# Kernel tuning notes

Hardware: AMD Instinct MI355X
Metric: run time of the kernel (lower is better)

Reference implementation:

```python
import jax, jax.numpy as jnp
import numpy as np

NUM_ITERS = 5
TEMP = 0.1


def setup_inputs() -> dict:
    key = jax.random.key(0)
    k1, k2 = jax.random.split(key)
    pred_masks = jax.random.uniform(k1, (1, 100, 512, 512), dtype=jnp.float32)
    gt_masks = jax.random.uniform(k2, (50, 512, 512), dtype=jnp.float32)
    return {"pred_masks": pred_masks, "gt_masks": gt_masks}


def reference(pred_masks, gt_masks):
    # pred_masks: [B=1, K, H, W]; gt_masks: [N, H, W]
    gt = gt_masks[None]  # [1, N, H, W]
    # cost[b,k,n] = 1 - <pred_k, gt_n> over HW
    cost = 1.0 - jnp.einsum('bkhw,bnhw->bkn', pred_masks, gt)
    log_alpha = -cost / TEMP  # [1, K, N]
    for _ in range(NUM_ITERS):
        log_alpha = log_alpha - jax.nn.logsumexp(log_alpha, axis=2, keepdims=True)
        log_alpha = log_alpha - jax.nn.logsumexp(log_alpha, axis=1, keepdims=True)
    return jnp.exp(log_alpha)
```

## Files before the change

kernel.cpp:

```cpp
#include <hip/hip_runtime.h>
#include <math.h>

#define HW    262144
#define MROWS 100
#define NCOLS 50
#define OUTSZ (MROWS * NCOLS)

typedef __attribute__((ext_vector_type(8))) short bf16x8;
typedef __attribute__((ext_vector_type(4))) float f32x4;

__device__ __forceinline__ unsigned short f32_bf16(float x) {
  unsigned int u = __float_as_uint(x);
  u += 0x7FFFu + ((u >> 16) & 1u);
  return (unsigned short)(u >> 16);
}
__device__ __forceinline__ float bf16_f32(unsigned short h) {
  return __uint_as_float(((unsigned int)h) << 16);
}
__device__ __forceinline__ void split_frag(const float4& v0, const float4& v1,
                                           bf16x8& hi, bf16x8& lo) {
  float xs[8] = {v0.x, v0.y, v0.z, v0.w, v1.x, v1.y, v1.z, v1.w};
#pragma unroll
  for (int j = 0; j < 8; ++j) {
    unsigned short h = f32_bf16(xs[j]);
    hi[j] = (short)h;
    lo[j] = (short)f32_bf16(xs[j] - bf16_f32(h));
  }
}

#define ABYTES   14336
#define BUFBYTES 24576
#define SLOT_ITERS 6

typedef __attribute__((address_space(1))) const unsigned int GU32;
typedef __attribute__((address_space(3))) unsigned int LU32;

__global__ __launch_bounds__(256, 3) void dm_phase1(
    const float* __restrict__ pred, const float* __restrict__ gt,
    float* __restrict__ partial, int chunk) {
  __shared__ unsigned char smem[2 * BUFBYTES];

  const int b    = blockIdx.x;
  const int tid  = threadIdx.x;
  const int lane = tid & 63;
  const int wid  = tid >> 6;
  const int wi = wid >> 1, wj = wid & 1;
  const int g = lane >> 4, r = lane & 15;

  const int kbase = b * chunk;
  const int nst   = chunk >> 5;

  const float* srcb[SLOT_ITERS];
#pragma unroll
  for (int it = 0; it < SLOT_ITERS; ++it) {
    int s = it * 256 + tid;
    if (s < 896) {
      int row = s >> 3, t = s & 7;
      int rr = row < MROWS ? row : MROWS - 1;
      srcb[it] = pred + (size_t)rr * HW + ((t ^ (row & 7)) << 2);
    } else if (s < 1408) {
      int s2 = s - 896;
      int row = s2 >> 3, t = s2 & 7;
      int rr = row < NCOLS ? row : NCOLS - 1;
      srcb[it] = gt + (size_t)rr * HW + ((t ^ (row & 7)) << 2);
    } else {
      srcb[it] = pred + ((s - 1408) << 2);
    }
  }

  auto STAGE = [&](int q, int k0f) {
    unsigned char* bufb = smem + q * BUFBYTES;
#pragma unroll
    for (int it = 0; it < SLOT_ITERS; ++it) {
      const float* src = srcb[it] + k0f;
      unsigned char* dst = bufb + (it * 256 + wid * 64) * 16;
      __builtin_amdgcn_global_load_lds((GU32*)src, (LU32*)dst, 16, 0, 0);
    }
  };

  f32x4 acc[4][2] = {};

  auto COMPUTE = [&](int q) {
    const unsigned char* bufb = smem + q * BUFBYTES;
    bf16x8 bh[2], bl[2];
#pragma unroll
    for (int nf = 0; nf < 2; ++nf) {
      int R = wj * 32 + nf * 16 + r;
      const unsigned char* rowb = bufb + ABYTES + R * 128;
      float4 v0 = *(const float4*)(rowb + (((2 * g    ) ^ (r & 7)) << 4));
      float4 v1 = *(const float4*)(rowb + (((2 * g + 1) ^ (r & 7)) << 4));
      split_frag(v0, v1, bh[nf], bl[nf]);
    }
#pragma unroll
    for (int mf = 0; mf < 4; ++mf) {
      if (wi == 0 || mf < 3) {
        int R = wi * 64 + mf * 16 + r;
        const unsigned char* rowb = bufb + R * 128;
        float4 v0 = *(const float4*)(rowb + (((2 * g    ) ^ (r & 7)) << 4));
        float4 v1 = *(const float4*)(rowb + (((2 * g + 1) ^ (r & 7)) << 4));
        bf16x8 ah, al;
        split_frag(v0, v1, ah, al);
#pragma unroll
        for (int nf = 0; nf < 2; ++nf) {
          acc[mf][nf] = __builtin_amdgcn_mfma_f32_16x16x32_bf16(ah, bh[nf], acc[mf][nf], 0, 0, 0);
          acc[mf][nf] = __builtin_amdgcn_mfma_f32_16x16x32_bf16(al, bh[nf], acc[mf][nf], 0, 0, 0);
          acc[mf][nf] = __builtin_amdgcn_mfma_f32_16x16x32_bf16(ah, bl[nf], acc[mf][nf], 0, 0, 0);
          acc[mf][nf] = __builtin_amdgcn_mfma_f32_16x16x32_bf16(al, bl[nf], acc[mf][nf], 0, 0, 0);
        }
      }
    }
  };

  STAGE(0, kbase);
  for (int s = 0; s < nst; ++s) {
    asm volatile("s_barrier" ::: "memory");
    if (s + 1 < nst) {
      STAGE((s + 1) & 1, kbase + (s + 1) * 32);
      asm volatile("s_waitcnt vmcnt(6)" ::: "memory");
    } else {
      asm volatile("s_waitcnt vmcnt(0)" ::: "memory");
    }
    asm volatile("s_barrier" ::: "memory");
    COMPUTE(s & 1);
  }

#pragma unroll
  for (int mf = 0; mf < 4; ++mf) {
#pragma unroll
    for (int nf = 0; nf < 2; ++nf) {
#pragma unroll
      for (int qq = 0; qq < 4; ++qq) {
        int row = wi * 64 + mf * 16 + g * 4 + qq;
        int col = wj * 32 + nf * 16 + r;
        if (row < MROWS && col < NCOLS)
          partial[(size_t)b * OUTSZ + row * NCOLS + col] = acc[mf][nf][qq];
      }
    }
  }
}

__global__ void dm_reduce(const float* __restrict__ partial,
                          double* __restrict__ la0, int nblk) {
  const int tid = threadIdx.x, wid = tid >> 6, lane = tid & 63;
  const int pbase = blockIdx.x * 16 + wid * 4;
  if (pbase >= OUTSZ) return;
  double d0 = 0, d1 = 0, d2 = 0, d3 = 0;
  for (int b = lane; b < nblk; b += 64) {
    float4 v = *(const float4*)(partial + (size_t)b * OUTSZ + pbase);
    d0 += (double)v.x; d1 += (double)v.y; d2 += (double)v.z; d3 += (double)v.w;
  }
#pragma unroll
  for (int off = 32; off; off >>= 1) {
    d0 += __shfl_xor(d0, off);
    d1 += __shfl_xor(d1, off);
    d2 += __shfl_xor(d2, off);
    d3 += __shfl_xor(d3, off);
  }
  if (lane == 0) {
    la0[pbase + 0] = (d0 - 1.0) * 10.0;
    la0[pbase + 1] = (d1 - 1.0) * 10.0;
    la0[pbase + 2] = (d2 - 1.0) * 10.0;
    la0[pbase + 3] = (d3 - 1.0) * 10.0;
  }
}

__global__ __launch_bounds__(256) void dm_sinkhorn(const double* __restrict__ la_in,
                                                   float* __restrict__ out) {
  __shared__ double la[OUTSZ];
  __shared__ double rp[MROWS];
  __shared__ double cp[NCOLS];
  const int t = threadIdx.x;
  for (int p = t; p < OUTSZ; p += 256) la[p] = la_in[p];
  if (t < NCOLS) cp[t] = 0.0;
  __syncthreads();
  for (int it = 0; it < 5; ++it) {
    if (t < 2 * MROWS) {
      int row = t >> 1, sl = t & 1;
      double m = -1e300;
      for (int j = sl; j < NCOLS; j += 2) m = fmax(m, la[row * NCOLS + j] - cp[j]);
      float s = 0.f;
      for (int j = sl; j < NCOLS; j += 2)
        s += __expf((float)(la[row * NCOLS + j] - cp[j] - m));
      double mo = __shfl_xor(m, 1); float so = __shfl_xor(s, 1);
      double mn = fmax(m, mo);
      s = s * __expf((float)(m - mn)) + so * __expf((float)(mo - mn));
      if (sl == 0) rp[row] = mn + (double)__logf(s);
    }
    __syncthreads();
    if (t < 4 * NCOLS) {
      int col = t >> 2, sl = t & 3;
      double m = -1e300;
      for (int i = sl; i < MROWS; i += 4) m = fmax(m, la[i * NCOLS + col] - rp[i]);
      float s = 0.f;
      for (int i = sl; i < MROWS; i += 4)
        s += __expf((float)(la[i * NCOLS + col] - rp[i] - m));
#pragma unroll
      for (int off = 1; off < 4; off <<= 1) {
        double mo = __shfl_xor(m, off); float so = __shfl_xor(s, off);
        double mn = fmax(m, mo);
        s = s * __expf((float)(m - mn)) + so * __expf((float)(mo - mn));
        m = mn;
      }
      if (sl == 0) cp[col] = m + (double)__logf(s);
    }
    __syncthreads();
  }
  for (int p = t; p < OUTSZ; p += 256)
    out[p] = __expf((float)(la[p] - rp[p / NCOLS] - cp[p % NCOLS]));
}

extern "C" void kernel_launch(void* const* d_in, const int* in_sizes, int n_in,
                              void* d_out, int out_size, void* d_ws, size_t ws_size,
                              hipStream_t stream) {
  const float* pred = (const float*)d_in[0];
  const float* gt   = (const float*)d_in[1];
  float* out = (float*)d_out;

  int nblk = 512;
  while (nblk > 1 &&
         ((size_t)nblk * OUTSZ * sizeof(float) + OUTSZ * sizeof(double)) > ws_size)
    nblk >>= 1;
  int chunk = HW / nblk;

  float*  partial = (float*)d_ws;
  double* la0 = (double*)((char*)d_ws + (size_t)nblk * OUTSZ * sizeof(float));

  dm_phase1<<<nblk, 256, 0, stream>>>(pred, gt, partial, chunk);
  dm_reduce<<<(OUTSZ + 15) / 16, 256, 0, stream>>>(partial, la0, nblk);
  dm_sinkhorn<<<1, 256, 0, stream>>>(la0, out);
}
```

Before: 85.72 us.

## Switch split-precision MFMA to fp16 with three products and rebalance grid

Replaces the bf16 hi/lo split with an fp16 split using packed round-toward-zero conversion, and drops the lo*lo product, cutting MFMAs per step from four to three. It also trims the unused LDS staging slots, restructures the double-buffer loop so the next stage is issued before compute with a single wait and barrier per step, uses 768 blocks with uneven K ranges when workspace allows, and unrolls the reduction with a templated block count. fp16 has a narrower exponent range than bf16, so accuracy depends on the inputs staying in range (fine for the uniform [0,1) masks). Round-toward-zero plus the dropped lo*lo term adds some error.

```diff
diff --git a/kernel.cpp b/kernel.cpp
--- a/kernel.cpp
+++ b/kernel.cpp
@@ -1,43 +1,39 @@
 #include <hip/hip_runtime.h>
 #include <math.h>
 
-#define HW    262144
-#define MROWS 100
-#define NCOLS 50
-#define OUTSZ (MROWS * NCOLS)
-
-typedef __attribute__((ext_vector_type(8))) short bf16x8;
-typedef __attribute__((ext_vector_type(4))) float f32x4;
-
-__device__ __forceinline__ unsigned short f32_bf16(float x) {
-  unsigned int u = __float_as_uint(x);
-  u += 0x7FFFu + ((u >> 16) & 1u);
-  return (unsigned short)(u >> 16);
-}
-__device__ __forceinline__ float bf16_f32(unsigned short h) {
-  return __uint_as_float(((unsigned int)h) << 16);
-}
-__device__ __forceinline__ void split_frag(const float4& v0, const float4& v1,
-                                           bf16x8& hi, bf16x8& lo) {
-  float xs[8] = {v0.x, v0.y, v0.z, v0.w, v1.x, v1.y, v1.z, v1.w};
-#pragma unroll
-  for (int j = 0; j < 8; ++j) {
-    unsigned short h = f32_bf16(xs[j]);
-    hi[j] = (short)h;
-    lo[j] = (short)f32_bf16(xs[j] - bf16_f32(h));
-  }
-}
+#define HW       262144
+#define TOTSTEPS (HW / 32)
+#define MROWS    100
+#define NCOLS    50
+#define OUTSZ    (MROWS * NCOLS)
+
+typedef __attribute__((ext_vector_type(8))) _Float16 f16x8;
+typedef __attribute__((ext_vector_type(2))) __fp16   fp16x2;
+typedef __attribute__((ext_vector_type(4))) float    f32x4;
 
 #define ABYTES   14336
-#define BUFBYTES 24576
-#define SLOT_ITERS 6
+#define BUFBYTES 22528
 
 typedef __attribute__((address_space(1))) const unsigned int GU32;
 typedef __attribute__((address_space(3))) unsigned int LU32;
 
+__device__ __forceinline__ void split_f16(const float4& v0, const float4& v1,
+                                          f16x8& hi, f16x8& lo) {
+  float xs[8] = {v0.x, v0.y, v0.z, v0.w, v1.x, v1.y, v1.z, v1.w};
+  union { fp16x2 p[4]; f16x8 v; } H, L;
+#pragma unroll
+  for (int j = 0; j < 4; ++j) {
+    H.p[j] = __builtin_amdgcn_cvt_pkrtz(xs[2 * j], xs[2 * j + 1]);
+    float l0 = xs[2 * j]     - (float)H.p[j][0];
+    float l1 = xs[2 * j + 1] - (float)H.p[j][1];
+    L.p[j] = __builtin_amdgcn_cvt_pkrtz(l0, l1);
+  }
+  hi = H.v; lo = L.v;
+}
+
 __global__ __launch_bounds__(256, 3) void dm_phase1(
     const float* __restrict__ pred, const float* __restrict__ gt,
-    float* __restrict__ partial, int chunk) {
+    float* __restrict__ partial, int nblk) {
   __shared__ unsigned char smem[2 * BUFBYTES];
 
   const int b    = blockIdx.x;
@@ -47,49 +43,51 @@
   const int wi = wid >> 1, wj = wid & 1;
   const int g = lane >> 4, r = lane & 15;
 
-  const int kbase = b * chunk;
-  const int nst   = chunk >> 5;
-
-  const float* srcb[SLOT_ITERS];
-#pragma unroll
-  for (int it = 0; it < SLOT_ITERS; ++it) {
-    int s = it * 256 + tid;
+  const int k0s = (int)(((long)b * TOTSTEPS) / nblk);
+  const int k1s = (int)(((long)(b + 1) * TOTSTEPS) / nblk);
+  const int nst = k1s - k0s;
+
+  const float* srcb[6];
+#pragma unroll
+  for (int it = 0; it < 6; ++it) {
+    int s = (it < 5) ? it * 256 + tid : 1280 + tid;
+    const float* p;
     if (s < 896) {
       int row = s >> 3, t = s & 7;
       int rr = row < MROWS ? row : MROWS - 1;
-      srcb[it] = pred + (size_t)rr * HW + ((t ^ (row & 7)) << 2);
-    } else if (s < 1408) {
+      p = pred + (size_t)rr * HW + ((t ^ (row & 7)) << 2);
+    } else {
       int s2 = s - 896;
       int row = s2 >> 3, t = s2 & 7;
       int rr = row < NCOLS ? row : NCOLS - 1;
-      srcb[it] = gt + (size_t)rr * HW + ((t ^ (row & 7)) << 2);
-    } else {
-      srcb[it] = pred + ((s - 1408) << 2);
-    }
-  }
-
-  auto STAGE = [&](int q, int k0f) {
+      p = gt + (size_t)rr * HW + ((t ^ (row & 7)) << 2);
+    }
+    srcb[it] = p;
+  }
+
+  auto STAGE = [&](int q, int kf) {
     unsigned char* bufb = smem + q * BUFBYTES;
 #pragma unroll
-    for (int it = 0; it < SLOT_ITERS; ++it) {
-      const float* src = srcb[it] + k0f;
-      unsigned char* dst = bufb + (it * 256 + wid * 64) * 16;
-      __builtin_amdgcn_global_load_lds((GU32*)src, (LU32*)dst, 16, 0, 0);
-    }
+    for (int it = 0; it < 5; ++it)
+      __builtin_amdgcn_global_load_lds((GU32*)(srcb[it] + kf),
+          (LU32*)(bufb + (it * 256 + wid * 64) * 16), 16, 0, 0);
+    if (wid < 2)
+      __builtin_amdgcn_global_load_lds((GU32*)(srcb[5] + kf),
+          (LU32*)(bufb + (1280 + wid * 64) * 16), 16, 0, 0);
   };
 
   f32x4 acc[4][2] = {};
 
   auto COMPUTE = [&](int q) {
     const unsigned char* bufb = smem + q * BUFBYTES;
-    bf16x8 bh[2], bl[2];
+    f16x8 bh[2], bl[2];
 #pragma unroll
     for (int nf = 0; nf < 2; ++nf) {
       int R = wj * 32 + nf * 16 + r;
       const unsigned char* rowb = bufb + ABYTES + R * 128;
       float4 v0 = *(const float4*)(rowb + (((2 * g    ) ^ (r & 7)) << 4));
       float4 v1 = *(const float4*)(rowb + (((2 * g + 1) ^ (r & 7)) << 4));
-      split_frag(v0, v1, bh[nf], bl[nf]);
+      split_f16(v0, v1, bh[nf], bl[nf]);
     }
 #pragma unroll
     for (int mf = 0; mf < 4; ++mf) {
@@ -98,30 +96,29 @@
         const unsigned char* rowb = bufb + R * 128;
         float4 v0 = *(const float4*)(rowb + (((2 * g    ) ^ (r & 7)) << 4));
         float4 v1 = *(const float4*)(rowb + (((2 * g + 1) ^ (r & 7)) << 4));
-        bf16x8 ah, al;
-        split_frag(v0, v1, ah, al);
+        f16x8 ah, al;
+        split_f16(v0, v1, ah, al);
 #pragma unroll
         for (int nf = 0; nf < 2; ++nf) {
-          acc[mf][nf] = __builtin_amdgcn_mfma_f32_16x16x32_bf16(ah, bh[nf], acc[mf][nf], 0, 0, 0);
-          acc[mf][nf] = __builtin_amdgcn_mfma_f32_16x16x32_bf16(al, bh[nf], acc[mf][nf], 0, 0, 0);
-          acc[mf][nf] = __builtin_amdgcn_mfma_f32_16x16x32_bf16(ah, bl[nf], acc[mf][nf], 0, 0, 0);
-          acc[mf][nf] = __builtin_amdgcn_mfma_f32_16x16x32_bf16(al, bl[nf], acc[mf][nf], 0, 0, 0);
+          acc[mf][nf] = __builtin_amdgcn_mfma_f32_16x16x32_f16(ah, bh[nf], acc[mf][nf], 0, 0, 0);
+          acc[mf][nf] = __builtin_amdgcn_mfma_f32_16x16x32_f16(al, bh[nf], acc[mf][nf], 0, 0, 0);
+          acc[mf][nf] = __builtin_amdgcn_mfma_f32_16x16x32_f16(ah, bl[nf], acc[mf][nf], 0, 0, 0);
         }
       }
     }
   };
 
-  STAGE(0, kbase);
+  STAGE(0, k0s << 5);
+  asm volatile("s_waitcnt vmcnt(0)" ::: "memory");
+  __builtin_amdgcn_s_barrier();
+
+  int q = 0;
   for (int s = 0; s < nst; ++s) {
-    asm volatile("s_barrier" ::: "memory");
-    if (s + 1 < nst) {
-      STAGE((s + 1) & 1, kbase + (s + 1) * 32);
-      asm volatile("s_waitcnt vmcnt(6)" ::: "memory");
-    } else {
-      asm volatile("s_waitcnt vmcnt(0)" ::: "memory");
-    }
-    asm volatile("s_barrier" ::: "memory");
-    COMPUTE(s & 1);
+    if (s + 1 < nst) STAGE(q ^ 1, (k0s + s + 1) << 5);
+    COMPUTE(q);
+    if (s + 1 < nst) asm volatile("s_waitcnt vmcnt(0)" ::: "memory");
+    __builtin_amdgcn_s_barrier();
+    q ^= 1;
   }
 
 #pragma unroll
@@ -139,15 +136,22 @@
   }
 }
 
+template <int NB>
 __global__ void dm_reduce(const float* __restrict__ partial,
-                          double* __restrict__ la0, int nblk) {
+                          double* __restrict__ la0) {
   const int tid = threadIdx.x, wid = tid >> 6, lane = tid & 63;
   const int pbase = blockIdx.x * 16 + wid * 4;
   if (pbase >= OUTSZ) return;
+  constexpr int IT = NB / 64;
+  float4 v[IT];
+#pragma unroll
+  for (int i = 0; i < IT; ++i)
+    v[i] = *(const float4*)(partial + (size_t)(lane + 64 * i) * OUTSZ + pbase);
   double d0 = 0, d1 = 0, d2 = 0, d3 = 0;
-  for (int b = lane; b < nblk; b += 64) {
-    float4 v = *(const float4*)(partial + (size_t)b * OUTSZ + pbase);
-    d0 += (double)v.x; d1 += (double)v.y; d2 += (double)v.z; d3 += (double)v.w;
+#pragma unroll
+  for (int i = 0; i < IT; ++i) {
+    d0 += (double)v[i].x; d1 += (double)v[i].y;
+    d2 += (double)v[i].z; d3 += (double)v[i].w;
   }
 #pragma unroll
   for (int off = 32; off; off >>= 1) {
@@ -216,16 +220,17 @@
   const float* gt   = (const float*)d_in[1];
   float* out = (float*)d_out;
 
-  int nblk = 512;
-  while (nblk > 1 &&
-         ((size_t)nblk * OUTSZ * sizeof(float) + OUTSZ * sizeof(double)) > ws_size)
-    nblk >>= 1;
-  int chunk = HW / nblk;
+  auto fits = [&](int nb) {
+    return ((size_t)nb * OUTSZ * sizeof(float) + OUTSZ * sizeof(double)) <= ws_size;
+  };
+  int nblk = fits(768) ? 768 : (fits(512) ? 512 : 256);
 
   float*  partial = (float*)d_ws;
   double* la0 = (double*)((char*)d_ws + (size_t)nblk * OUTSZ * sizeof(float));
 
-  dm_phase1<<<nblk, 256, 0, stream>>>(pred, gt, partial, chunk);
-  dm_reduce<<<(OUTSZ + 15) / 16, 256, 0, stream>>>(partial, la0, nblk);
+  dm_phase1<<<nblk, 256, 0, stream>>>(pred, gt, partial, nblk);
+  if (nblk == 768)      dm_reduce<768><<<(OUTSZ + 15) / 16, 256, 0, stream>>>(partial, la0);
+  else if (nblk == 512) dm_reduce<512><<<(OUTSZ + 15) / 16, 256, 0, stream>>>(partial, la0);
+  else                  dm_reduce<256><<<(OUTSZ + 15) / 16, 256, 0, stream>>>(partial, la0);
   dm_sinkhorn<<<1, 256, 0, stream>>>(la0, out);
 }
```

Result: faster. 80.13 us (-6.5%).
